# Kernel tuning notes

Measured on AMD Instinct MI355X. Metric: run time of the kernel, lower is better.

Reference implementation:

```python
import jax, jax.numpy as jnp
import numpy as np

VOCAB, D_IN, D_H = 32000, 512, 1024
B, T = 16, 256
PAD_IDX = 0


def setup_inputs() -> dict:
    key = jax.random.key(0)
    k1, k2, k3, k4, k5 = jax.random.split(key, 5)
    input_idx = jax.random.randint(k1, (B, T), 0, VOCAB, dtype=jnp.int64)
    emb = jax.random.normal(k2, (VOCAB, D_IN), dtype=jnp.float32) * 0.02
    emb = emb.at[PAD_IDX].set(0.0)  # padding_idx row is zero
    weight_x = jax.random.normal(k3, (D_H, D_IN), dtype=jnp.float32) * (1.0 / np.sqrt(D_IN))
    weight_h = jax.random.normal(k4, (D_H, D_H), dtype=jnp.float32) * (1.0 / np.sqrt(D_H))
    bias = jnp.zeros((D_H,), dtype=jnp.float32)
    lm_W = jax.random.normal(k5, (VOCAB, D_H), dtype=jnp.float32) * (1.0 / np.sqrt(D_H))
    return {"input_idx": input_idx, "emb": emb, "weight_x": weight_x,
            "weight_h": weight_h, "bias": bias, "lm_W": lm_W}


def reference(input_idx, emb, weight_x, weight_h, bias, lm_W):
    Bsz = input_idx.shape[0]
    h0 = jnp.zeros((Bsz, weight_h.shape[0]), dtype=weight_x.dtype)

    def step(h, tok):
        x = emb[tok]  # [B, D_IN]
        h_new = jnp.tanh(x @ weight_x.T + h @ weight_h.T + bias)
        mask = (tok != PAD_IDX)[:, None]  # keep old h at pad positions
        h = jnp.where(mask, h_new, h)
        return h, h

    _, h_all = jax.lax.scan(step, h0, input_idx.T)  # [T, B, H]
    h_all = jnp.swapaxes(h_all, 0, 1)               # [B, T, H]
    logits = jnp.einsum('bth,vh->btv', h_all, lm_W)  # [B, T, V]
    return logits
```

## Files before the change

kernel.cpp:

```cpp
#include <hip/hip_runtime.h>

#define PAD_IDX 0

typedef __attribute__((ext_vector_type(8))) short short8;
typedef __attribute__((ext_vector_type(4))) float f32x4;

__device__ __forceinline__ unsigned short f32_to_bf16_rne(float f) {
  unsigned int u = __builtin_bit_cast(unsigned int, f);
  u += 0x7FFFu + ((u >> 16) & 1u);
  return (unsigned short)(u >> 16);
}

__device__ __forceinline__ void load16_to_lds(const void* g, void* lds) {
  __builtin_amdgcn_global_load_lds(
      (const __attribute__((address_space(1))) unsigned int*)g,
      (__attribute__((address_space(3))) unsigned int*)lds,
      16, 0, 0);
}

__global__ void sentinel_kernel(float* out) { out[0] = 1.0e6f; }

__global__ __launch_bounds__(256) void xwcvt_kernel(const int* __restrict__ tok,
                                                    const float* __restrict__ emb,
                                                    const float* __restrict__ Wx,
                                                    const float* __restrict__ bias,
                                                    float* __restrict__ xw,
                                                    const float* __restrict__ lmW,
                                                    unsigned short* __restrict__ lmW_bf) {
  int tid = threadIdx.x;
  if (blockIdx.x >= 1024) {
    const int n8 = 32000 * 1024 / 8;
    int stride = 512 * 256;
    for (int i = (blockIdx.x - 1024) * 256 + tid; i < n8; i += stride) {
      float4 a = ((const float4*)lmW)[2 * i];
      float4 b = ((const float4*)lmW)[2 * i + 1];
      ushort4 lo, hi;
      lo.x = f32_to_bf16_rne(a.x); lo.y = f32_to_bf16_rne(a.y);
      lo.z = f32_to_bf16_rne(a.z); lo.w = f32_to_bf16_rne(a.w);
      hi.x = f32_to_bf16_rne(b.x); hi.y = f32_to_bf16_rne(b.y);
      hi.z = f32_to_bf16_rne(b.z); hi.w = f32_to_bf16_rne(b.w);
      ((ushort4*)lmW_bf)[2 * i] = lo;
      ((ushort4*)lmW_bf)[2 * i + 1] = hi;
    }
    return;
  }
  __shared__ float At[32][68];
  __shared__ float Bt[32][68];
  __shared__ int stok[64];
  int tm = blockIdx.x & 63;
  int tn = blockIdx.x >> 6;
  int r0 = tm * 64, j0 = tn * 64;
  if (tid < 64) stok[tid] = tok[r0 + tid];
  int tx = tid & 15, ty = tid >> 4;
  float acc[4][4] = {};
  for (int kt = 0; kt < 512; kt += 32) {
    __syncthreads();
    #pragma unroll
    for (int ii = 0; ii < 2; ++ii) {
      int idx = tid * 2 + ii;
      int m = idx >> 3, fv = idx & 7;
      float4 va = *(const float4*)&emb[(size_t)stok[m] * 512 + kt + fv * 4];
      float4 vb = *(const float4*)&Wx[(size_t)(j0 + m) * 512 + kt + fv * 4];
      At[fv * 4 + 0][m] = va.x; At[fv * 4 + 1][m] = va.y;
      At[fv * 4 + 2][m] = va.z; At[fv * 4 + 3][m] = va.w;
      Bt[fv * 4 + 0][m] = vb.x; Bt[fv * 4 + 1][m] = vb.y;
      Bt[fv * 4 + 2][m] = vb.z; Bt[fv * 4 + 3][m] = vb.w;
    }
    __syncthreads();
    #pragma unroll
    for (int k = 0; k < 32; ++k) {
      float4 a4 = *(const float4*)&At[k][ty * 4];
      float4 b4 = *(const float4*)&Bt[k][tx * 4];
      float av[4] = {a4.x, a4.y, a4.z, a4.w};
      float bv[4] = {b4.x, b4.y, b4.z, b4.w};
      #pragma unroll
      for (int i = 0; i < 4; ++i)
        #pragma unroll
        for (int jj = 0; jj < 4; ++jj) acc[i][jj] = fmaf(av[i], bv[jj], acc[i][jj]);
    }
  }
  #pragma unroll
  for (int i = 0; i < 4; ++i) {
    size_t row = (size_t)(r0 + ty * 4 + i) * 1024 + j0 + tx * 4;
    #pragma unroll
    for (int jj = 0; jj < 4; ++jj)
      xw[row + jj] = acc[i][jj] + bias[j0 + tx * 4 + jj];
  }
}

__global__ __launch_bounds__(1024, 4) void rec_kernel(const float* __restrict__ Wh,
                                                      const float* __restrict__ xw,
                                                      const int* __restrict__ tok,
                                                      unsigned long long* hcomb,
                                                      unsigned short* __restrict__ h_all) {
  int c = blockIdx.x & 15;
  int g = blockIdx.x >> 4;
  int tid = threadIdx.x;
  int w = tid >> 6;
  int l = tid & 63;
  int j = g * 64 + l;

  const float* wb = Wh + (size_t)j * 1024 + w * 64;
#define LDW(i) f32x4 w##i = *(const f32x4*)(wb + i * 4);
  LDW(0) LDW(1) LDW(2) LDW(3) LDW(4) LDW(5) LDW(6) LDW(7)
  LDW(8) LDW(9) LDW(10) LDW(11) LDW(12) LDW(13) LDW(14) LDW(15)
#undef LDW

  __shared__ float hs[16][64];
  __shared__ float pbuf[16][64];
  unsigned long long* hc0 = hcomb + (size_t)c * 1024;
  unsigned long long* hc1 = hcomb + 16 * 1024 + (size_t)c * 1024;
  bool writer = (w == 0);
  float prevh = 0.f;

  for (int t = 0; t < 256; ++t) {
    float xv = 0.f;
    int tkn = 1;
    if (writer) {
      xv = xw[((size_t)c * 256 + t) * 1024 + j];
      tkn = tok[c * 256 + t];
    }
    unsigned long long* src = ((t & 1) ? hc1 : hc0) + tid;
    unsigned long long v;
    int guard = 0;
    do {
      v = __hip_atomic_load(src, __ATOMIC_RELAXED, __HIP_MEMORY_SCOPE_AGENT);
      if ((unsigned int)(v >> 32) == (unsigned int)t) break;
      __builtin_amdgcn_s_sleep(1);
    } while (++guard < (1 << 20));
    hs[w][l] = __builtin_bit_cast(float, (unsigned int)v);
    __asm__ volatile("s_waitcnt lgkmcnt(0)" ::: "memory");

    const float* hp = &hs[w][0];
    f32x4 a0 = {0.f, 0.f, 0.f, 0.f}, a1 = a0, a2 = a0, a3 = a0;
#define FMAI(i, acc) { f32x4 h4 = *(const f32x4*)(hp + i * 4); acc += w##i * h4; }
    FMAI(0, a0) FMAI(1, a1) FMAI(2, a2) FMAI(3, a3)
    FMAI(4, a0) FMAI(5, a1) FMAI(6, a2) FMAI(7, a3)
    FMAI(8, a0) FMAI(9, a1) FMAI(10, a2) FMAI(11, a3)
    FMAI(12, a0) FMAI(13, a1) FMAI(14, a2) FMAI(15, a3)
#undef FMAI
    f32x4 aa = (a0 + a1) + (a2 + a3);
    pbuf[w][l] = (aa[0] + aa[1]) + (aa[2] + aa[3]);
    __asm__ volatile("s_waitcnt lgkmcnt(0)\n\ts_barrier" ::: "memory");

    if (writer) {
      float s = 0.f;
      #pragma unroll
      for (int q = 0; q < 16; ++q) s += pbuf[q][l];
      float hnew;
      if (tkn != PAD_IDX) {
        float pre = xv + s;
        float e = __builtin_amdgcn_exp2f(pre * 2.8853900817779268f);
        hnew = 1.0f - 2.0f / (e + 1.0f);
      } else {
        hnew = prevh;
      }
      prevh = hnew;
      unsigned long long pv =
          ((unsigned long long)(unsigned int)(t + 1) << 32) |
          (unsigned long long)__builtin_bit_cast(unsigned int, hnew);
      __hip_atomic_store((((t + 1) & 1) ? hc1 : hc0) + j, pv,
                         __ATOMIC_RELAXED, __HIP_MEMORY_SCOPE_AGENT);
      h_all[((size_t)c * 256 + t) * 1024 + j] = f32_to_bf16_rne(hnew);
    }
  }
}

__global__ __launch_bounds__(512) void gemm_kernel(const unsigned short* __restrict__ A,
                                                   const unsigned short* __restrict__ B,
                                                   float* __restrict__ C) {
  __shared__ unsigned short lds[2 * 32768];
  int tid = threadIdx.x;
  int lane = tid & 63, wave = tid >> 6;
  int bid = blockIdx.x;
  int x = bid & 7;
  int r = bid >> 3;
  int tm = 2 * x + (r & 1);
  int tn = r >> 1;
  int r0 = tm * 256, c0 = tn * 256;
  int wm = wave >> 2, wn = wave & 3;

  auto SH = [&](int kt, int st, int mat, int half) {
    unsigned short* buf = (unsigned short*)lds + st * 32768 + mat * 16384 + half * 8192;
    const unsigned short* src = mat ? (B + (size_t)(c0 + half * 128) * 1024)
                                    : (A + (size_t)(r0 + half * 128) * 1024);
    #pragma unroll
    for (int i = 0; i < 2; ++i) {
      int slot = i * 512 + tid;
      int row = slot >> 3, sg = slot & 7;
      int kg = sg ^ (row & 7);
      const unsigned short* g = src + (size_t)row * 1024 + kt * 64 + kg * 8;
      load16_to_lds(g, &buf[(i * 512 + wave * 64) * 8]);
    }
  };

  f32x4 zero = {0.f, 0.f, 0.f, 0.f};
  f32x4 acc[8][4];
  #pragma unroll
  for (int i = 0; i < 8; ++i)
    #pragma unroll
    for (int jx = 0; jx < 4; ++jx) acc[i][jx] = zero;

  SH(0, 0, 0, 0); SH(0, 0, 0, 1); SH(0, 0, 1, 0); SH(0, 0, 1, 1);
  SH(1, 1, 0, 0); SH(1, 1, 0, 1);
  __asm__ volatile("s_waitcnt vmcnt(0)" ::: "memory");
  __builtin_amdgcn_s_barrier();

  for (int kt = 0; kt < 16; ++kt) {
    int st = kt & 1;
    const char* bufA = (const char*)((const unsigned short*)lds + st * 32768);
    const char* bufB = bufA + 32768;
    int ktB = kt + 1 > 15 ? 15 : kt + 1;
    int ktA = kt + 2 > 15 ? 15 : kt + 2;
    int kb0 = (lane >> 4) * 16;
    int kb1 = 64 + kb0;
    short8 af0[8], af1[8], bf0[4], bf1[4];

    #pragma unroll
    for (int i = 0; i < 8; ++i) {
      int rowa = wm * 128 + i * 16 + (lane & 15);
      af0[i] = *(const short8*)(bufA + rowa * 128 + (kb0 ^ ((rowa & 7) << 4)));
    }
    #pragma unroll
    for (int jx = 0; jx < 2; ++jx) {
      int rowb = wn * 64 + jx * 16 + (lane & 15);
      bf0[jx] = *(const short8*)(bufB + rowb * 128 + (kb0 ^ ((rowb & 7) << 4)));
    }
    SH(ktB, st ^ 1, 1, 0);
    __builtin_amdgcn_s_barrier();
    __asm__ volatile("s_waitcnt lgkmcnt(0)" ::: "memory");
    __builtin_amdgcn_s_setprio(1);
    #pragma unroll
    for (int i = 0; i < 8; ++i)
      #pragma unroll
      for (int jx = 0; jx < 2; ++jx)
        acc[i][jx] = __builtin_amdgcn_mfma_f32_16x16x32_bf16(af0[i], bf0[jx], acc[i][jx], 0, 0, 0);
    __builtin_amdgcn_s_setprio(0);
    __builtin_amdgcn_s_barrier();

    #pragma unroll
    for (int jx = 2; jx < 4; ++jx) {
      int rowb = wn * 64 + jx * 16 + (lane & 15);
      bf0[jx] = *(const short8*)(bufB + rowb * 128 + (kb0 ^ ((rowb & 7) << 4)));
    }
    SH(ktB, st ^ 1, 1, 1);
    __builtin_amdgcn_s_barrier();
    __asm__ volatile("s_waitcnt lgkmcnt(0)" ::: "memory");
    __builtin_amdgcn_s_setprio(1);
    #pragma unroll
    for (int i = 0; i < 8; ++i)
      #pragma unroll
      for (int jx = 2; jx < 4; ++jx)
        acc[i][jx] = __builtin_amdgcn_mfma_f32_16x16x32_bf16(af0[i], bf0[jx], acc[i][jx], 0, 0, 0);
    __builtin_amdgcn_s_setprio(0);
    __builtin_amdgcn_s_barrier();

    #pragma unroll
    for (int i = 0; i < 8; ++i) {
      int rowa = wm * 128 + i * 16 + (lane & 15);
      af1[i] = *(const short8*)(bufA + rowa * 128 + (kb1 ^ ((rowa & 7) << 4)));
    }
    #pragma unroll
    for (int jx = 0; jx < 2; ++jx) {
      int rowb = wn * 64 + jx * 16 + (lane & 15);
      bf1[jx] = *(const short8*)(bufB + rowb * 128 + (kb1 ^ ((rowb & 7) << 4)));
    }
    __builtin_amdgcn_s_barrier();
    __asm__ volatile("s_waitcnt lgkmcnt(0)" ::: "memory");
    __builtin_amdgcn_s_setprio(1);
    #pragma unroll
    for (int i = 0; i < 8; ++i)
      #pragma unroll
      for (int jx = 0; jx < 2; ++jx)
        acc[i][jx] = __builtin_amdgcn_mfma_f32_16x16x32_bf16(af1[i], bf1[jx], acc[i][jx], 0, 0, 0);
    __builtin_amdgcn_s_setprio(0);
    __builtin_amdgcn_s_barrier();

    #pragma unroll
    for (int jx = 2; jx < 4; ++jx) {
      int rowb = wn * 64 + jx * 16 + (lane & 15);
      bf1[jx] = *(const short8*)(bufB + rowb * 128 + (kb1 ^ ((rowb & 7) << 4)));
    }
    SH(ktA, st, 0, 0);
    SH(ktA, st, 0, 1);
    __builtin_amdgcn_s_barrier();
    __asm__ volatile("s_waitcnt lgkmcnt(0)" ::: "memory");
    __builtin_amdgcn_s_setprio(1);
    #pragma unroll
    for (int i = 0; i < 8; ++i)
      #pragma unroll
      for (int jx = 2; jx < 4; ++jx)
        acc[i][jx] = __builtin_amdgcn_mfma_f32_16x16x32_bf16(af1[i], bf1[jx], acc[i][jx], 0, 0, 0);
    __builtin_amdgcn_s_setprio(0);
    __asm__ volatile("s_waitcnt vmcnt(4)" ::: "memory");
    __builtin_amdgcn_s_barrier();
  }
  __asm__ volatile("s_waitcnt vmcnt(0)" ::: "memory");

  int rbase = r0 + wm * 128 + (lane >> 4) * 4;
  int cbase = c0 + wn * 64 + (lane & 15);
  #pragma unroll
  for (int i = 0; i < 8; ++i)
    #pragma unroll
    for (int jx = 0; jx < 4; ++jx)
      #pragma unroll
      for (int q = 0; q < 4; ++q)
        C[(size_t)(rbase + i * 16 + q) * 32000 + cbase + jx * 16] = acc[i][jx][q];
}

extern "C" void kernel_launch(void* const* d_in, const int* in_sizes, int n_in,
                              void* d_out, int out_size, void* d_ws, size_t ws_size,
                              hipStream_t stream) {
  const int* tok = (const int*)d_in[0];
  const float* emb = (const float*)d_in[1];
  const float* Wx = (const float*)d_in[2];
  const float* Wh = (const float*)d_in[3];
  const float* bias = (const float*)d_in[4];
  const float* lmW = (const float*)d_in[5];
  float* out = (float*)d_out;

  const size_t OFF_LMW = 0;
  const size_t OFF_XW = 65536000;
  const size_t OFF_HALL = OFF_XW + 16777216;
  const size_t OFF_HCMB = OFF_HALL + 8388608;
  const size_t NEED = OFF_HCMB + 262144;
  if (ws_size < NEED) {
    sentinel_kernel<<<1, 1, 0, stream>>>(out);
    return;
  }
  char* ws = (char*)d_ws;
  unsigned short* lmW_bf = (unsigned short*)(ws + OFF_LMW);
  float* xw = (float*)(ws + OFF_XW);
  unsigned short* h_all = (unsigned short*)(ws + OFF_HALL);
  unsigned long long* hcomb = (unsigned long long*)(ws + OFF_HCMB);

  hipMemsetAsync(ws + OFF_HCMB, 0, 262144, stream);
  xwcvt_kernel<<<1536, 256, 0, stream>>>(tok, emb, Wx, bias, xw, lmW, lmW_bf);
  rec_kernel<<<256, 1024, 0, stream>>>(Wh, xw, tok, hcomb, h_all);
  gemm_kernel<<<2000, 512, 0, stream>>>(h_all, lmW_bf, out);
}
```

Baseline: 868.4 us.

## Fuse input projection and lm_W bf16 conversion into the recurrent kernel

Removes the separate xwcvt kernel and the memset. Each recurrent block now does three things before its time loop: it computes its own 256x64 tile of emb[tok]·Wx^T + bias into LDS, it converts a grid-strided slice of lm_W to bf16, and it zeroes its slice of the h-exchange buffer. This drops the global xw round trip, one kernel launch and the memset. In exchange the recurrent kernel gets a longer serial prologue using scalar FMAs, and LDS use rises to about 72KB. The in-kernel zeroing of the exchange buffer is not ordered across blocks, so a stale tag left by a previous call could be read.

```diff
diff --git a/kernel.cpp b/kernel.cpp
--- a/kernel.cpp
+++ b/kernel.cpp
@@ -20,18 +20,63 @@
 
 __global__ void sentinel_kernel(float* out) { out[0] = 1.0e6f; }
 
-__global__ __launch_bounds__(256) void xwcvt_kernel(const int* __restrict__ tok,
-                                                    const float* __restrict__ emb,
-                                                    const float* __restrict__ Wx,
-                                                    const float* __restrict__ bias,
-                                                    float* __restrict__ xw,
-                                                    const float* __restrict__ lmW,
-                                                    unsigned short* __restrict__ lmW_bf) {
+__global__ __launch_bounds__(1024, 4) void rec_kernel(const float* __restrict__ Wh,
+                                                      const int* __restrict__ tok,
+                                                      const float* __restrict__ emb,
+                                                      const float* __restrict__ Wx,
+                                                      const float* __restrict__ bias,
+                                                      const float* __restrict__ lmW,
+                                                      unsigned short* __restrict__ lmW_bf,
+                                                      unsigned long long* hcomb,
+                                                      unsigned short* __restrict__ h_all) {
+  int c = blockIdx.x & 15;
+  int g = blockIdx.x >> 4;
   int tid = threadIdx.x;
-  if (blockIdx.x >= 1024) {
+  int w = tid >> 6;
+  int l = tid & 63;
+  int j = g * 64 + l;
+
+  __shared__ float xwtile[256 * 64];
+  __shared__ float hs[16][64];
+  __shared__ float pbuf[16][64];
+
+  if (tid < 128) {
+    int p = tid >> 6, jj0 = g * 64 + (tid & 63);
+    __hip_atomic_store(hcomb + (size_t)p * 16384 + c * 1024 + jj0, 0ull,
+                       __ATOMIC_RELAXED, __HIP_MEMORY_SCOPE_AGENT);
+  }
+
+  {
+    int jp = tid & 63;
+    int tg = tid >> 6;
+    int jj = g * 64 + jp;
+    const float* wxrow = Wx + (size_t)jj * 512;
+    float bv = bias[jj];
+    int toks[16];
+    #pragma unroll
+    for (int s = 0; s < 16; ++s) toks[s] = tok[c * 256 + tg * 16 + s];
+    float ax[16];
+    #pragma unroll
+    for (int s = 0; s < 16; ++s) ax[s] = bv;
+    for (int kc = 0; kc < 512; kc += 4) {
+      f32x4 wv = *(const f32x4*)(wxrow + kc);
+      #pragma unroll
+      for (int s = 0; s < 16; ++s) {
+        f32x4 ev = *(const f32x4*)(emb + (size_t)toks[s] * 512 + kc);
+        ax[s] = fmaf(wv[0], ev[0], ax[s]);
+        ax[s] = fmaf(wv[1], ev[1], ax[s]);
+        ax[s] = fmaf(wv[2], ev[2], ax[s]);
+        ax[s] = fmaf(wv[3], ev[3], ax[s]);
+      }
+    }
+    #pragma unroll
+    for (int s = 0; s < 16; ++s) xwtile[(tg * 16 + s) * 64 + jp] = ax[s];
+  }
+
+  {
     const int n8 = 32000 * 1024 / 8;
-    int stride = 512 * 256;
-    for (int i = (blockIdx.x - 1024) * 256 + tid; i < n8; i += stride) {
+    int gstride = 256 * 1024;
+    for (int i = blockIdx.x * 1024 + tid; i < n8; i += gstride) {
       float4 a = ((const float4*)lmW)[2 * i];
       float4 b = ((const float4*)lmW)[2 * i + 1];
       ushort4 lo, hi;
@@ -42,63 +87,8 @@
       ((ushort4*)lmW_bf)[2 * i] = lo;
       ((ushort4*)lmW_bf)[2 * i + 1] = hi;
     }
-    return;
-  }
-  __shared__ float At[32][68];
-  __shared__ float Bt[32][68];
-  __shared__ int stok[64];
-  int tm = blockIdx.x & 63;
-  int tn = blockIdx.x >> 6;
-  int r0 = tm * 64, j0 = tn * 64;
-  if (tid < 64) stok[tid] = tok[r0 + tid];
-  int tx = tid & 15, ty = tid >> 4;
-  float acc[4][4] = {};
-  for (int kt = 0; kt < 512; kt += 32) {
-    __syncthreads();
-    #pragma unroll
-    for (int ii = 0; ii < 2; ++ii) {
-      int idx = tid * 2 + ii;
-      int m = idx >> 3, fv = idx & 7;
-      float4 va = *(const float4*)&emb[(size_t)stok[m] * 512 + kt + fv * 4];
-      float4 vb = *(const float4*)&Wx[(size_t)(j0 + m) * 512 + kt + fv * 4];
-      At[fv * 4 + 0][m] = va.x; At[fv * 4 + 1][m] = va.y;
-      At[fv * 4 + 2][m] = va.z; At[fv * 4 + 3][m] = va.w;
-      Bt[fv * 4 + 0][m] = vb.x; Bt[fv * 4 + 1][m] = vb.y;
-      Bt[fv * 4 + 2][m] = vb.z; Bt[fv * 4 + 3][m] = vb.w;
-    }
-    __syncthreads();
-    #pragma unroll
-    for (int k = 0; k < 32; ++k) {
-      float4 a4 = *(const float4*)&At[k][ty * 4];
-      float4 b4 = *(const float4*)&Bt[k][tx * 4];
-      float av[4] = {a4.x, a4.y, a4.z, a4.w};
-      float bv[4] = {b4.x, b4.y, b4.z, b4.w};
-      #pragma unroll
-      for (int i = 0; i < 4; ++i)
-        #pragma unroll
-        for (int jj = 0; jj < 4; ++jj) acc[i][jj] = fmaf(av[i], bv[jj], acc[i][jj]);
-    }
-  }
-  #pragma unroll
-  for (int i = 0; i < 4; ++i) {
-    size_t row = (size_t)(r0 + ty * 4 + i) * 1024 + j0 + tx * 4;
-    #pragma unroll
-    for (int jj = 0; jj < 4; ++jj)
-      xw[row + jj] = acc[i][jj] + bias[j0 + tx * 4 + jj];
-  }
-}
-
-__global__ __launch_bounds__(1024, 4) void rec_kernel(const float* __restrict__ Wh,
-                                                      const float* __restrict__ xw,
-                                                      const int* __restrict__ tok,
-                                                      unsigned long long* hcomb,
-                                                      unsigned short* __restrict__ h_all) {
-  int c = blockIdx.x & 15;
-  int g = blockIdx.x >> 4;
-  int tid = threadIdx.x;
-  int w = tid >> 6;
-  int l = tid & 63;
-  int j = g * 64 + l;
+  }
+  __syncthreads();
 
   const float* wb = Wh + (size_t)j * 1024 + w * 64;
 #define LDW(i) f32x4 w##i = *(const f32x4*)(wb + i * 4);
@@ -106,8 +96,6 @@
   LDW(8) LDW(9) LDW(10) LDW(11) LDW(12) LDW(13) LDW(14) LDW(15)
 #undef LDW
 
-  __shared__ float hs[16][64];
-  __shared__ float pbuf[16][64];
   unsigned long long* hc0 = hcomb + (size_t)c * 1024;
   unsigned long long* hc1 = hcomb + 16 * 1024 + (size_t)c * 1024;
   bool writer = (w == 0);
@@ -117,7 +105,7 @@
     float xv = 0.f;
     int tkn = 1;
     if (writer) {
-      xv = xw[((size_t)c * 256 + t) * 1024 + j];
+      xv = xwtile[t * 64 + l];
       tkn = tok[c * 256 + t];
     }
     unsigned long long* src = ((t & 1) ? hc1 : hc0) + tid;
@@ -320,8 +308,7 @@
   float* out = (float*)d_out;
 
   const size_t OFF_LMW = 0;
-  const size_t OFF_XW = 65536000;
-  const size_t OFF_HALL = OFF_XW + 16777216;
+  const size_t OFF_HALL = 65536000;
   const size_t OFF_HCMB = OFF_HALL + 8388608;
   const size_t NEED = OFF_HCMB + 262144;
   if (ws_size < NEED) {
@@ -330,12 +317,10 @@
   }
   char* ws = (char*)d_ws;
   unsigned short* lmW_bf = (unsigned short*)(ws + OFF_LMW);
-  float* xw = (float*)(ws + OFF_XW);
   unsigned short* h_all = (unsigned short*)(ws + OFF_HALL);
   unsigned long long* hcomb = (unsigned long long*)(ws + OFF_HCMB);
 
-  hipMemsetAsync(ws + OFF_HCMB, 0, 262144, stream);
-  xwcvt_kernel<<<1536, 256, 0, stream>>>(tok, emb, Wx, bias, xw, lmW, lmW_bf);
-  rec_kernel<<<256, 1024, 0, stream>>>(Wh, xw, tok, hcomb, h_all);
+  rec_kernel<<<256, 1024, 0, stream>>>(Wh, tok, emb, Wx, bias, lmW, lmW_bf,
+                                       hcomb, h_all);
   gemm_kernel<<<2000, 512, 0, stream>>>(h_all, lmW_bf, out);
 }
```

Result: slower. 1.119 ms (+28.8%).
